# Performance work log

Measured on AMD Instinct MI355X. Metric: run time of the kernel, lower is better.

The kernel has to match this reference:

```python
import jax, jax.numpy as jnp
import numpy as np

BS, M, CLIP_DIM = 64, 1000, 512
D = 512
N_WAYS = 20
N_Z = 8


def setup_inputs() -> dict:
    key = jax.random.key(0)
    ks = jax.random.split(key, 16)
    s = 0.02
    inp = {
        "x_context": jax.random.normal(ks[0], (BS, M, CLIP_DIM), jnp.float32),
        "y_context": jax.random.randint(ks[1], (BS, M), 0, N_WAYS),
        "x_query": jax.random.normal(ks[2], (BS, M, CLIP_DIM), jnp.float32),
        # image_proj
        "Wp": jax.random.normal(ks[3], (CLIP_DIM, D), jnp.float32) * s,
        "bp": jnp.zeros((D,), jnp.float32),
        # aggregator: Linear(d,d) -> GELU -> Linear(d,2d)
        "Wa1": jax.random.normal(ks[4], (D, D), jnp.float32) * s,
        "ba1": jnp.zeros((D,), jnp.float32),
        "Wa2": jax.random.normal(ks[5], (D, 2 * D), jnp.float32) * s,
        "ba2": jnp.zeros((2 * D,), jnp.float32),
        # decoder: Linear(d,d) -> GELU -> Linear(d,d)
        "Wd1": jax.random.normal(ks[6], (D, D), jnp.float32) * s,
        "bd1": jnp.zeros((D,), jnp.float32),
        "Wd2": jax.random.normal(ks[7], (D, D), jnp.float32) * s,
        "bd2": jnp.zeros((D,), jnp.float32),
    }
    return inp


def reference(x_context, y_context, x_query, Wp, bp, Wa1, ba1, Wa2, ba2, Wd1, bd1, Wd2, bd2):
    # project image embeddings: [bs, M, clip_dim] -> [bs, M, d]
    xc = x_context @ Wp + bp
    xq = x_query @ Wp + bp

    # encode_context_per_class: per-class masked sum == one-hot segment-sum
    # (original loops over classes doing (x*mask).sum(dim=1))
    oh = jax.nn.one_hot(y_context, N_WAYS, dtype=xc.dtype)  # [bs, M, N]
    r_C = jnp.einsum('bmn,bmd->bnd', oh, xc)  # [bs, N, d]

    # knowledge is None -> k = zeros; combined = relu(r + 0)
    combined = jax.nn.relu(r_C)
    h = jax.nn.gelu(combined @ Wa1 + ba1, approximate=False)
    stats = h @ Wa2 + ba2  # [bs, N, 2d]
    mu, scale_raw = stats[..., :D], stats[..., D:]
    scale = 0.01 + 0.99 * jax.nn.softplus(scale_raw)

    # eval path: sample n_z from q(z|C) via reparameterization
    eps = jax.random.normal(jax.random.key(42), (N_Z,) + mu.shape, mu.dtype)
    z_samples = mu[None] + scale[None] * eps  # [n_z, bs, N, d]

    # decode: class weight vectors then inner product with queries
    W = jax.nn.gelu(z_samples @ Wd1 + bd1, approximate=False) @ Wd2 + bd2
    logits = jnp.einsum('bqd,sbnd->sbqn', xq, W)  # [n_z, bs, Q*N, N]
    return logits, z_samples, mu, scale
```

## Files before the change

### kernel.cpp

```cpp
#include <hip/hip_runtime.h>
#include <hip/hip_bf16.h>
#include <stdint.h>


typedef __attribute__((ext_vector_type(8))) short short8;
typedef __attribute__((ext_vector_type(4))) float f32x4;

__device__ __forceinline__ float gelu_f(float x) {
    return 0.5f * x * (1.0f + erff(x * 0.70710678118654752440f));
}
__device__ __forceinline__ float softplus_f(float x) {
    return fmaxf(x, 0.0f) + log1pf(expf(-fabsf(x)));
}
__device__ __forceinline__ uint32_t cvt2(float a, float b) {
    __hip_bfloat162 h;
    h.x = __float2bfloat16(a);
    h.y = __float2bfloat16(b);
    uint32_t u; __builtin_memcpy(&u, &h, 4); return u;
}
__device__ __forceinline__ unsigned short f2bfu(float f) {
    __hip_bfloat16 h = __float2bfloat16(f);
    unsigned short u; __builtin_memcpy(&u, &h, 2); return u;
}
__device__ __forceinline__ float bfu2f(unsigned short u) {
    uint32_t v = (uint32_t)u << 16; float f; __builtin_memcpy(&f, &v, 4); return f;
}

__device__ __forceinline__ void threefry2x32(uint32_t k0, uint32_t k1,
                                             uint32_t x0, uint32_t x1,
                                             uint32_t& o0, uint32_t& o1) {
    uint32_t ks[3] = {k0, k1, k0 ^ k1 ^ 0x1BD11BDAu};
    x0 += ks[0]; x1 += ks[1];
    const uint32_t rot[8] = {13,15,26,6,17,29,16,24};
#pragma unroll
    for (int i = 0; i < 5; i++) {
#pragma unroll
        for (int j = 0; j < 4; j++) {
            uint32_t r = rot[(i & 1) * 4 + j];
            x0 += x1;
            x1 = (x1 << r) | (x1 >> (32 - r));
            x1 ^= x0;
        }
        x0 += ks[(i + 1) % 3];
        x1 += ks[(i + 2) % 3] + (uint32_t)(i + 1);
    }
    o0 = x0; o1 = x1;
}

__device__ __forceinline__ float bits_to_normal(uint32_t b) {
    float f = __uint_as_float((b >> 9) | 0x3F800000u) - 1.0f;
    const float lo = __uint_as_float(0xBF7FFFFFu);
    float u = fmaxf(lo, f * 2.0f + lo);
    return 1.41421356237309504880f * erfinvf(u);
}

__global__ __launch_bounds__(256) void prep_k(
    const float* __restrict__ Wp, const float* __restrict__ Wa1,
    const float* __restrict__ Wa2, const float* __restrict__ Wd1,
    const float* __restrict__ Wd2, const float* __restrict__ bp,
    const float* __restrict__ bd2, const int* __restrict__ y,
    unsigned short* __restrict__ WpTb, unsigned short* __restrict__ Wa1Tb,
    unsigned short* __restrict__ Wa2Tb, unsigned short* __restrict__ WdT1b,
    float* __restrict__ bv, float* __restrict__ w2bp,
    float* __restrict__ c0, float* __restrict__ cnt)
{
    __shared__ float T[64][65];
    __shared__ int lc[32];
    __shared__ float ws4[4];
    const int f = blockIdx.x;
    const int tid = threadIdx.x;

    if (f < 320) {
        const float* src; unsigned short* dst; int C, t, xb, yb;
        if (f < 64)       { src = Wp;  dst = WpTb;  C = 512;  t = f;       xb = t & 7;  yb = t >> 3; }
        else if (f < 128) { src = Wa1; dst = Wa1Tb; C = 512;  t = f - 64;  xb = t & 7;  yb = t >> 3; }
        else if (f < 256) { src = Wa2; dst = Wa2Tb; C = 1024; t = f - 128; xb = t & 15; yb = t >> 4; }
        else              { src = Wd1; dst = WdT1b; C = 512;  t = f - 256; xb = t & 7;  yb = t >> 3; }
        const int r0 = yb * 64, cc0 = xb * 64;
        const int rr = tid >> 4, cc = (tid & 15) * 4;
#pragma unroll
        for (int l = 0; l < 4; l++) {
            int row = rr + l * 16;
            float4 v = *(const float4*)&src[(size_t)(r0 + row) * C + cc0 + cc];
            T[row][cc] = v.x; T[row][cc+1] = v.y; T[row][cc+2] = v.z; T[row][cc+3] = v.w;
        }
        __syncthreads();
#pragma unroll
        for (int l = 0; l < 4; l++) {
            int n = rr + l * 16;
            uint2 u;
            u.x = cvt2(T[cc][n], T[cc+1][n]);
            u.y = cvt2(T[cc+2][n], T[cc+3][n]);
            *(uint2*)&dst[(size_t)(cc0 + n) * 512 + r0 + cc] = u;
        }
    } else if (f < 576) {
        const float* W = (f < 448) ? Wp : Wd2;
        const float* v = (f < 448) ? bd2 : bp;
        float* o = (f < 448) ? bv : w2bp;
        int t = (f < 448) ? f - 320 : f - 448;
        int wave = tid >> 6, lane = tid & 63;
        int r = t * 4 + wave;
        const float* row = W + (size_t)r * 512 + lane * 8;
        float4 x0 = *(const float4*)row;
        float4 x1 = *(const float4*)(row + 4);
        float4 v0 = *(const float4*)&v[lane * 8];
        float4 v1 = *(const float4*)&v[lane * 8 + 4];
        float s = x0.x*v0.x + x0.y*v0.y + x0.z*v0.z + x0.w*v0.w
                + x1.x*v1.x + x1.y*v1.y + x1.z*v1.z + x1.w*v1.w;
#pragma unroll
        for (int off = 32; off > 0; off >>= 1) s += __shfl_down(s, off, 64);
        if (lane == 0) o[r] = s;
    } else if (f == 576) {
        float s = bp[tid] * bd2[tid] + bp[tid + 256] * bd2[tid + 256];
#pragma unroll
        for (int off = 32; off > 0; off >>= 1) s += __shfl_down(s, off, 64);
        int wave = tid >> 6, lane = tid & 63;
        if (lane == 0) ws4[wave] = s;
        __syncthreads();
        if (tid == 0) c0[0] = ws4[0] + ws4[1] + ws4[2] + ws4[3];
    } else {
        int b = f - 577;
        if (tid < 32) lc[tid] = 0;
        __syncthreads();
        for (int m = tid; m < 1000; m += 256)
            atomicAdd(&lc[y[b * 1000 + m]], 1);
        __syncthreads();
        if (tid < 20) cnt[b * 20 + tid] = (float)lc[tid];
    }
}

__global__ __launch_bounds__(256) void gmG_k(const float* __restrict__ Ap,
                                             const float* __restrict__ Bp,
                                             unsigned short* __restrict__ C) {
    __shared__ unsigned short As[64 * 64];
    __shared__ unsigned short Bs[128 * 64];
    const int tid = threadIdx.x;
    const int lane = tid & 63, w = tid >> 6;
    const int row0 = blockIdx.y * 64, col0 = blockIdx.x * 128;
    f32x4 acc[4][2] = {};
    for (int k0 = 0; k0 < 512; k0 += 64) {
        {
            int row = tid >> 2, cs = (tid & 3) * 16;
            int swz = (row & 7) << 4;
            const float* src = Ap + (size_t)(row0 + row) * 512 + k0 + cs;
#pragma unroll
            for (int j = 0; j < 2; j++) {
                float4 v0 = *(const float4*)(src + j * 8);
                float4 v1 = *(const float4*)(src + j * 8 + 4);
                uint4 u;
                u.x = cvt2(v0.x, v0.y); u.y = cvt2(v0.z, v0.w);
                u.z = cvt2(v1.x, v1.y); u.w = cvt2(v1.z, v1.w);
                *(uint4*)((char*)As + row * 128 + (((cs + j * 8) * 2) ^ swz)) = u;
            }
        }
        {
            int row = tid >> 1, cs = (tid & 1) * 32;
            int swz = (row & 7) << 4;
            const float* src = Bp + (size_t)(col0 + row) * 512 + k0 + cs;
#pragma unroll
            for (int j = 0; j < 4; j++) {
                float4 v0 = *(const float4*)(src + j * 8);
                float4 v1 = *(const float4*)(src + j * 8 + 4);
                uint4 u;
                u.x = cvt2(v0.x, v0.y); u.y = cvt2(v0.z, v0.w);
                u.z = cvt2(v1.x, v1.y); u.w = cvt2(v1.z, v1.w);
                *(uint4*)((char*)Bs + row * 128 + (((cs + j * 8) * 2) ^ swz)) = u;
            }
        }
        __syncthreads();
#pragma unroll
        for (int ks = 0; ks < 2; ks++) {
            short8 a[4], bb[2];
#pragma unroll
            for (int mi = 0; mi < 4; mi++) {
                int r = mi * 16 + (lane & 15);
                a[mi] = *(const short8*)((const char*)As + r * 128 +
                          (((ks * 32 + (lane >> 4) * 8) * 2) ^ ((r & 7) << 4)));
            }
#pragma unroll
            for (int ni = 0; ni < 2; ni++) {
                int n = w * 32 + ni * 16 + (lane & 15);
                bb[ni] = *(const short8*)((const char*)Bs + n * 128 +
                          (((ks * 32 + (lane >> 4) * 8) * 2) ^ ((n & 7) << 4)));
            }
#pragma unroll
            for (int mi = 0; mi < 4; mi++)
#pragma unroll
                for (int ni = 0; ni < 2; ni++)
                    acc[mi][ni] = __builtin_amdgcn_mfma_f32_16x16x32_bf16(a[mi], bb[ni], acc[mi][ni], 0, 0, 0);
        }
        __syncthreads();
    }
#pragma unroll
    for (int mi = 0; mi < 4; mi++)
#pragma unroll
        for (int ni = 0; ni < 2; ni++) {
            int c = col0 + w * 32 + ni * 16 + (lane & 15);
#pragma unroll
            for (int j = 0; j < 4; j++) {
                int r = row0 + mi * 16 + (lane >> 4) * 4 + j;
                C[(size_t)r * 512 + c] = f2bfu(acc[mi][ni][j]);
            }
        }
}

__global__ __launch_bounds__(256) void onehot4_k(const float* __restrict__ xc,
                                                 const int* __restrict__ y,
                                                 float* __restrict__ Apart) {
    __shared__ unsigned short Xs[128 * 64];
    __shared__ int ys[256];
    const int chb = blockIdx.x * 128;
    const int mc = blockIdx.y;
    const int b = blockIdx.z;
    const int m00 = mc * 256;
    const int tid = threadIdx.x, lane = tid & 63, w = tid >> 6;
    const int chs = w * 32;

    {
        int mg = m00 + tid;
        ys[tid] = (mg < 1000) ? y[b * 1000 + mg] : -1;
    }

    f32x4 acc[2][2] = {};
    for (int step = 0; step < 4; step++) {
        const int k0 = step * 64;
        int m = m00 + k0 + lane; if (m > 999) m = 999;
        const float* src = xc + ((size_t)b * 1000 + m) * 512 + chb + chs;
        float x[32];
#pragma unroll
        for (int j8 = 0; j8 < 8; j8++) {
            float4 v = *(const float4*)(src + j8 * 4);
            x[j8*4+0]=v.x; x[j8*4+1]=v.y; x[j8*4+2]=v.z; x[j8*4+3]=v.w;
        }
        __syncthreads();
#pragma unroll
        for (int j = 0; j < 32; j++) {
            int ch = chs + j;
            *(unsigned short*)((char*)Xs + ch * 128 + ((lane * 2) ^ ((ch & 7) << 4)))
                = f2bfu(x[j]);
        }
        __syncthreads();
#pragma unroll
        for (int ks = 0; ks < 2; ks++) {
            int kb = ks * 32 + (lane >> 4) * 8;
            int4 yv0 = *(const int4*)&ys[k0 + kb];
            int4 yv1 = *(const int4*)&ys[k0 + kb + 4];
            int ya[8] = {yv0.x, yv0.y, yv0.z, yv0.w, yv1.x, yv1.y, yv1.z, yv1.w};
            short8 a[2];
#pragma unroll
            for (int mi = 0; mi < 2; mi++) {
                int cls = mi * 16 + (lane & 15);
#pragma unroll
                for (int e = 0; e < 8; e++)
                    a[mi][e] = (short)((ya[e] == cls) ? 0x3F80 : 0);
            }
            short8 bb[2];
#pragma unroll
            for (int ni = 0; ni < 2; ni++) {
                int ch = chs + ni * 16 + (lane & 15);
                bb[ni] = *(const short8*)((const char*)Xs + ch * 128 +
                           ((kb * 2) ^ ((ch & 7) << 4)));
            }
#pragma unroll
            for (int mi = 0; mi < 2; mi++)
#pragma unroll
                for (int ni = 0; ni < 2; ni++)
                    acc[mi][ni] = __builtin_amdgcn_mfma_f32_16x16x32_bf16(a[mi], bb[ni], acc[mi][ni], 0, 0, 0);
        }
    }
    float* dst = Apart + (size_t)mc * 655360;
#pragma unroll
    for (int mi = 0; mi < 2; mi++) {
#pragma unroll
        for (int ni = 0; ni < 2; ni++) {
            int ch = chb + chs + ni * 16 + (lane & 15);
#pragma unroll
            for (int j = 0; j < 4; j++) {
                int cls = mi * 16 + (lane >> 4) * 4 + j;
                if (cls < 20)
                    dst[((size_t)b * 20 + cls) * 512 + ch] = acc[mi][ni][j];
            }
        }
    }
}

__global__ __launch_bounds__(256) void reduceA_k(const float* __restrict__ Apart,
                                                 unsigned short* __restrict__ Abf) {
    int i = blockIdx.x * 256 + threadIdx.x;
    if (i < 163840) {
        const float4* Ap4 = (const float4*)Apart;
        float4 s = Ap4[i];
#pragma unroll
        for (int p = 1; p < 4; p++) {
            float4 v = Ap4[(size_t)p * 163840 + i];
            s.x += v.x; s.y += v.y; s.z += v.z; s.w += v.w;
        }
        uint2 o;
        o.x = cvt2(s.x, s.y); o.y = cvt2(s.z, s.w);
        *(uint2*)&Abf[(size_t)i * 4] = o;
    }
}

template <int EPI>
__global__ __launch_bounds__(256) void gm2_k(const unsigned short* __restrict__ Abf,
                                             const unsigned short* __restrict__ Bbf,
                                             const float* __restrict__ bias,
                                             const float* __restrict__ extra,
                                             unsigned short* __restrict__ C0,
                                             float* __restrict__ F0,
                                             float* __restrict__ F1,
                                             int Nn) {
    __shared__ unsigned short As[64 * 64];
    __shared__ unsigned short Bs[128 * 64];
    const int tid = threadIdx.x;
    const int lane = tid & 63, w = tid >> 6;
    const int row0 = blockIdx.y * 64, col0 = blockIdx.x * 128;
    f32x4 acc[4][2] = {};
    for (int k0 = 0; k0 < 512; k0 += 64) {
        {
            int row = tid >> 2, cs = (tid & 3) * 16;
            int swz = (row & 7) << 4;
            const unsigned short* src = Abf + (size_t)(row0 + row) * 512 + k0 + cs;
#pragma unroll
            for (int j = 0; j < 2; j++) {
                uint4 u = *(const uint4*)(src + j * 8);
                *(uint4*)((char*)As + row * 128 + (((cs + j * 8) * 2) ^ swz)) = u;
            }
        }
        {
            int row = tid >> 1, cs = (tid & 1) * 32;
            int swz = (row & 7) << 4;
            const unsigned short* src = Bbf + (size_t)(col0 + row) * 512 + k0 + cs;
#pragma unroll
            for (int j = 0; j < 4; j++) {
                uint4 u = *(const uint4*)(src + j * 8);
                *(uint4*)((char*)Bs + row * 128 + (((cs + j * 8) * 2) ^ swz)) = u;
            }
        }
        __syncthreads();
#pragma unroll
        for (int ks = 0; ks < 2; ks++) {
            short8 a[4], bb[2];
#pragma unroll
            for (int mi = 0; mi < 4; mi++) {
                int r = mi * 16 + (lane & 15);
                a[mi] = *(const short8*)((const char*)As + r * 128 +
                          (((ks * 32 + (lane >> 4) * 8) * 2) ^ ((r & 7) << 4)));
            }
#pragma unroll
            for (int ni = 0; ni < 2; ni++) {
                int n = w * 32 + ni * 16 + (lane & 15);
                bb[ni] = *(const short8*)((const char*)Bs + n * 128 +
                          (((ks * 32 + (lane >> 4) * 8) * 2) ^ ((n & 7) << 4)));
            }
#pragma unroll
            for (int mi = 0; mi < 4; mi++)
#pragma unroll
                for (int ni = 0; ni < 2; ni++)
                    acc[mi][ni] = __builtin_amdgcn_mfma_f32_16x16x32_bf16(a[mi], bb[ni], acc[mi][ni], 0, 0, 0);
        }
        __syncthreads();
    }
#pragma unroll
    for (int mi = 0; mi < 4; mi++) {
#pragma unroll
        for (int ni = 0; ni < 2; ni++) {
            int c = col0 + w * 32 + ni * 16 + (lane & 15);
            float bvv = bias ? bias[c] : 0.f;
#pragma unroll
            for (int j = 0; j < 4; j++) {
                int r = row0 + mi * 16 + (lane >> 4) * 4 + j;
                float v = acc[mi][ni][j];
                if (EPI == 0) {
                    v += bvv;
                    C0[(size_t)r * Nn + c] = f2bfu(v);
                } else if (EPI == 1) {
                    v += extra[r] * bvv;
                    C0[(size_t)r * Nn + c] = f2bfu(fmaxf(v, 0.f));
                } else if (EPI == 2) {
                    C0[(size_t)r * Nn + c] = f2bfu(gelu_f(v + bvv));
                } else {
                    v += bvv;
                    if (c < 512) F0[(size_t)r * 512 + c] = v;
                    else F1[(size_t)r * 512 + (c - 512)] = 0.01f + 0.99f * softplus_f(v);
                }
            }
        }
    }
}

__global__ __launch_bounds__(256) void z2_k(const float* __restrict__ mu,
                                            const float* __restrict__ sc,
                                            float* __restrict__ z,
                                            unsigned short* __restrict__ zb) {
    const uint32_t NH = 2621440u;
    uint32_t i = blockIdx.x * 256u + threadIdx.x;
    if (i >= NH) return;
    uint32_t t0 = 2u * i;
    uint32_t o0, o1, p0, p1;
    threefry2x32(0u, 42u, 0u, t0, o0, o1);
    threefry2x32(0u, 42u, 0u, t0 + 1u, p0, p1);
    uint32_t r0 = t0 % 655360u;
    float2 mv = *(const float2*)&mu[r0];
    float2 sv = *(const float2*)&sc[r0];
    float z0 = mv.x + sv.x * bits_to_normal(o0 ^ o1);
    float z1 = mv.y + sv.y * bits_to_normal(p0 ^ p1);
    float2 zo; zo.x = z0; zo.y = z1;
    *(float2*)&z[t0] = zo;
    *(uint32_t*)&zb[t0] = cvt2(z0, z1);
}

__global__ __launch_bounds__(256) void beta2_k(const unsigned short* __restrict__ Wgb,
                                               const float* __restrict__ vec,
                                               const float* __restrict__ c0,
                                               float* __restrict__ beta) {
    int wave = threadIdx.x >> 6, lane = threadIdx.x & 63;
    int r = blockIdx.x * 4 + wave;
    short8 wv = *(const short8*)(Wgb + (size_t)r * 512 + lane * 8);
    float s = 0.f;
#pragma unroll
    for (int e = 0; e < 8; e++) s += vec[lane * 8 + e] * bfu2f((unsigned short)wv[e]);
#pragma unroll
    for (int o = 32; o > 0; o >>= 1) s += __shfl_down(s, o, 64);
    if (lane == 0) beta[r] = s + c0[0];
}

__global__ __launch_bounds__(512) void logits_mfma3_k(const float* __restrict__ Xq,
                                                      const unsigned short* __restrict__ Vb,
                                                      const float* __restrict__ beta,
                                                      float* __restrict__ out) {
    __shared__ unsigned short Vs[160 * 64];
    __shared__ float bs[160];
    const int u = blockIdx.x + 8 * blockIdx.y;
    const int xcd = u & 7, idx = u >> 3;
    const int b = (idx & 7) * 8 + xcd;
    const int qh = idx >> 3;
    const int tid = threadIdx.x, lane = tid & 63, w = tid >> 6;
    const int wq = w >> 1, wn = w & 1;

    if (tid < 160) {
        int s = tid / 20, n = tid - s * 20;
        bs[tid] = beta[(size_t)(s * 64 + b) * 20 + n];
    }

    const int klane = (lane >> 4) * 8;
    const float* xp[2];
    int qb[2];
#pragma unroll
    for (int qs = 0; qs < 2; qs++) {
        qb[qs] = qh * 128 + wq * 32 + qs * 16;
        int qr = qb[qs] + (lane & 15);
        if (qr > 999) qr = 999;
        xp[qs] = Xq + ((size_t)b * 1000 + qr) * 512 + klane;
    }
    int vrow[5], vswz[5];
#pragma unroll
    for (int nf = 0; nf < 5; nf++) {
        int rr = wn * 80 + nf * 16 + (lane & 15);
        vrow[nf] = rr * 128;
        vswz[nf] = (rr & 7) << 4;
    }

    f32x4 acc[2][5] = {};
    for (int k0 = 0; k0 < 512; k0 += 64) {
        __syncthreads();
        for (int c = tid; c < 640; c += 512) {
            int row = c >> 2, off = (c & 3) * 32;
            int sdiv = row / 20;
            int row_g = row + sdiv * 1260 + b * 20;
            const unsigned short* src = Vb + (size_t)row_g * 512 + k0 + (c & 3) * 16;
            uint4 u0 = *(const uint4*)src;
            uint4 u1 = *(const uint4*)(src + 8);
            int swz = (row & 7) << 4;
            char* base = (char*)Vs + row * 128;
            *(uint4*)(base + (off ^ swz)) = u0;
            *(uint4*)(base + ((off + 16) ^ swz)) = u1;
        }
        __syncthreads();
#pragma unroll
        for (int ks = 0; ks < 2; ks++) {
            int kb = (ks * 32 + klane) * 2;
            short8 bf[5];
#pragma unroll
            for (int nf = 0; nf < 5; nf++)
                bf[nf] = *(const short8*)((const char*)Vs + vrow[nf] + (kb ^ vswz[nf]));
            short8 af[2];
#pragma unroll
            for (int qs = 0; qs < 2; qs++) {
                const float* p = xp[qs] + k0 + ks * 32;
                float4 v0 = *(const float4*)p;
                float4 v1 = *(const float4*)(p + 4);
                uint4 uu;
                uu.x = cvt2(v0.x, v0.y); uu.y = cvt2(v0.z, v0.w);
                uu.z = cvt2(v1.x, v1.y); uu.w = cvt2(v1.z, v1.w);
                __builtin_memcpy(&af[qs], &uu, 16);
            }
#pragma unroll
            for (int qs = 0; qs < 2; qs++)
#pragma unroll
                for (int nf = 0; nf < 5; nf++)
                    acc[qs][nf] = __builtin_amdgcn_mfma_f32_16x16x32_bf16(af[qs], bf[nf], acc[qs][nf], 0, 0, 0);
        }
    }

#pragma unroll
    for (int nf = 0; nf < 5; nf++) {
        int rl = wn * 80 + nf * 16 + (lane & 15);
        int s = rl / 20, n = rl - s * 20;
        float bb = bs[rl];
        size_t ob = (size_t)(s * 64 + b) * 20000;
#pragma unroll
        for (int qs = 0; qs < 2; qs++) {
#pragma unroll
            for (int j = 0; j < 4; j++) {
                int q = qb[qs] + (lane >> 4) * 4 + j;
                if (q < 1000)
                    out[ob + (size_t)q * 20 + n] = acc[qs][nf][j] + bb;
            }
        }
    }
}

extern "C" void kernel_launch(void* const* d_in, const int* in_sizes, int n_in,
                              void* d_out, int out_size, void* d_ws, size_t ws_size,
                              hipStream_t stream) {
    const float* x_context = (const float*)d_in[0];
    const int*   y_context = (const int*)d_in[1];
    const float* x_query   = (const float*)d_in[2];
    const float* Wp  = (const float*)d_in[3];
    const float* bp  = (const float*)d_in[4];
    const float* Wa1 = (const float*)d_in[5];
    const float* ba1 = (const float*)d_in[6];
    const float* Wa2 = (const float*)d_in[7];
    const float* ba2 = (const float*)d_in[8];
    const float* Wd1 = (const float*)d_in[9];
    const float* bd1 = (const float*)d_in[10];
    const float* Wd2 = (const float*)d_in[11];
    const float* bd2 = (const float*)d_in[12];

    float* out    = (float*)d_out;
    float* logits = out;
    float* z      = out + 10240000;
    float* mu     = out + 15482880;
    float* sc     = out + 16138240;

    float* ws   = (float*)d_ws;
    float* cnt  = ws;
    float* beta = cnt + 1280;
    float* bv   = beta + 10240;
    float* w2bp = bv + 512;
    float* c0   = w2bp + 512;
    unsigned short* WpTb  = (unsigned short*)(c0 + 63);
    unsigned short* Wa1Tb = WpTb + 262144;
    unsigned short* Wa2Tb = Wa1Tb + 262144;
    unsigned short* WdT1b = Wa2Tb + 524288;
    unsigned short* Gtb   = WdT1b + 262144;
    unsigned short* Abf   = Gtb + 262144;
    unsigned short* combb = Abf + 655360;
    unsigned short* hb    = combb + 655360;
    unsigned short* zb    = hb + 655360;
    unsigned short* Vbf   = zb + 5242880;
    float* big = (float*)(Vbf + 5242880);
    unsigned short* Wgb = (unsigned short*)big;

    prep_k<<<dim3(641), 256, 0, stream>>>(Wp, Wa1, Wa2, Wd1, Wd2, bp, bd2, y_context,
                                          WpTb, Wa1Tb, Wa2Tb, WdT1b,
                                          bv, w2bp, c0, cnt);
    gmG_k<<<dim3(4, 8), 256, 0, stream>>>(Wp, Wd2, Gtb);
    onehot4_k<<<dim3(4, 4, 64), 256, 0, stream>>>(x_context, y_context, big);
    reduceA_k<<<dim3(640), 256, 0, stream>>>(big, Abf);
    gm2_k<1><<<dim3(4, 20), 256, 0, stream>>>(Abf, WpTb, bp, cnt, combb, nullptr, nullptr, 512);
    gm2_k<2><<<dim3(4, 20), 256, 0, stream>>>(combb, Wa1Tb, ba1, nullptr, hb, nullptr, nullptr, 512);
    gm2_k<3><<<dim3(8, 20), 256, 0, stream>>>(hb, Wa2Tb, ba2, nullptr, nullptr, mu, sc, 1024);
    z2_k<<<dim3(10240), 256, 0, stream>>>(mu, sc, z, zb);
    gm2_k<2><<<dim3(4, 160), 256, 0, stream>>>(zb, WdT1b, bd1, nullptr, Wgb, nullptr, nullptr, 512);
    gm2_k<0><<<dim3(4, 160), 256, 0, stream>>>(Wgb, Gtb, bv, nullptr, Vbf, nullptr, nullptr, 512);
    beta2_k<<<dim3(2560), 256, 0, stream>>>(Wgb, w2bp, c0, beta);
    logits_mfma3_k<<<dim3(8, 64), 512, 0, stream>>>(x_query, Vbf, beta, logits);
}
```

Measured before the change: 236.0 us.

## Fuse gmG into prep, fold partial-sum reduce into GEMM, double-buffer logits V tiles

The Wp·Wd2 product GEMM now runs as extra blocks inside the prep kernel, and the reduceA kernel is removed. The first small-M GEMM now sums the four fp32 partials directly while staging its A tile. The small-M GEMMs use 32-row tiles so more blocks run across the 1280-row problems. The logits kernel double-buffers its V tile in shared memory, so the next k-slice loads while the current one is multiplied, which removes one barrier per step. Together these cut two launches and one intermediate round trip, at the cost of more shared memory and redundant partial reads per column block.

```diff
diff --git a/kernel.cpp b/kernel.cpp
--- a/kernel.cpp
+++ b/kernel.cpp
@@ -61,16 +61,18 @@
     const float* __restrict__ bd2, const int* __restrict__ y,
     unsigned short* __restrict__ WpTb, unsigned short* __restrict__ Wa1Tb,
     unsigned short* __restrict__ Wa2Tb, unsigned short* __restrict__ WdT1b,
+    unsigned short* __restrict__ Gtb,
     float* __restrict__ bv, float* __restrict__ w2bp,
     float* __restrict__ c0, float* __restrict__ cnt)
 {
-    __shared__ float T[64][65];
+    __shared__ __align__(16) char sm[24576];
     __shared__ int lc[32];
     __shared__ float ws4[4];
     const int f = blockIdx.x;
     const int tid = threadIdx.x;
 
     if (f < 320) {
+        float (*T)[65] = reinterpret_cast<float(*)[65]>(sm);
         const float* src; unsigned short* dst; int C, t, xb, yb;
         if (f < 64)       { src = Wp;  dst = WpTb;  C = 512;  t = f;       xb = t & 7;  yb = t >> 3; }
         else if (f < 128) { src = Wa1; dst = Wa1Tb; C = 512;  t = f - 64;  xb = t & 7;  yb = t >> 3; }
@@ -118,7 +120,7 @@
         if (lane == 0) ws4[wave] = s;
         __syncthreads();
         if (tid == 0) c0[0] = ws4[0] + ws4[1] + ws4[2] + ws4[3];
-    } else {
+    } else if (f < 641) {
         int b = f - 577;
         if (tid < 32) lc[tid] = 0;
         __syncthreads();
@@ -126,82 +128,78 @@
             atomicAdd(&lc[y[b * 1000 + m]], 1);
         __syncthreads();
         if (tid < 20) cnt[b * 20 + tid] = (float)lc[tid];
-    }
-}
-
-__global__ __launch_bounds__(256) void gmG_k(const float* __restrict__ Ap,
-                                             const float* __restrict__ Bp,
-                                             unsigned short* __restrict__ C) {
-    __shared__ unsigned short As[64 * 64];
-    __shared__ unsigned short Bs[128 * 64];
-    const int tid = threadIdx.x;
-    const int lane = tid & 63, w = tid >> 6;
-    const int row0 = blockIdx.y * 64, col0 = blockIdx.x * 128;
-    f32x4 acc[4][2] = {};
-    for (int k0 = 0; k0 < 512; k0 += 64) {
-        {
-            int row = tid >> 2, cs = (tid & 3) * 16;
-            int swz = (row & 7) << 4;
-            const float* src = Ap + (size_t)(row0 + row) * 512 + k0 + cs;
-#pragma unroll
-            for (int j = 0; j < 2; j++) {
-                float4 v0 = *(const float4*)(src + j * 8);
-                float4 v1 = *(const float4*)(src + j * 8 + 4);
-                uint4 u;
-                u.x = cvt2(v0.x, v0.y); u.y = cvt2(v0.z, v0.w);
-                u.z = cvt2(v1.x, v1.y); u.w = cvt2(v1.z, v1.w);
-                *(uint4*)((char*)As + row * 128 + (((cs + j * 8) * 2) ^ swz)) = u;
-            }
-        }
-        {
-            int row = tid >> 1, cs = (tid & 1) * 32;
-            int swz = (row & 7) << 4;
-            const float* src = Bp + (size_t)(col0 + row) * 512 + k0 + cs;
-#pragma unroll
-            for (int j = 0; j < 4; j++) {
-                float4 v0 = *(const float4*)(src + j * 8);
-                float4 v1 = *(const float4*)(src + j * 8 + 4);
-                uint4 u;
-                u.x = cvt2(v0.x, v0.y); u.y = cvt2(v0.z, v0.w);
-                u.z = cvt2(v1.x, v1.y); u.w = cvt2(v1.z, v1.w);
-                *(uint4*)((char*)Bs + row * 128 + (((cs + j * 8) * 2) ^ swz)) = u;
-            }
-        }
-        __syncthreads();
-#pragma unroll
-        for (int ks = 0; ks < 2; ks++) {
-            short8 a[4], bb[2];
-#pragma unroll
-            for (int mi = 0; mi < 4; mi++) {
-                int r = mi * 16 + (lane & 15);
-                a[mi] = *(const short8*)((const char*)As + r * 128 +
-                          (((ks * 32 + (lane >> 4) * 8) * 2) ^ ((r & 7) << 4)));
-            }
+    } else {
+        unsigned short* As = (unsigned short*)sm;
+        unsigned short* Bs = (unsigned short*)(sm + 8192);
+        const int g = f - 641;
+        const int lane = tid & 63, w = tid >> 6;
+        const int row0 = (g >> 2) * 64, col0 = (g & 3) * 128;
+        f32x4 acc[4][2] = {};
+        for (int k0 = 0; k0 < 512; k0 += 64) {
+            {
+                int row = tid >> 2, cs = (tid & 3) * 16;
+                int swz = (row & 7) << 4;
+                const float* src = Wp + (size_t)(row0 + row) * 512 + k0 + cs;
+#pragma unroll
+                for (int j = 0; j < 2; j++) {
+                    float4 v0 = *(const float4*)(src + j * 8);
+                    float4 v1 = *(const float4*)(src + j * 8 + 4);
+                    uint4 u;
+                    u.x = cvt2(v0.x, v0.y); u.y = cvt2(v0.z, v0.w);
+                    u.z = cvt2(v1.x, v1.y); u.w = cvt2(v1.z, v1.w);
+                    *(uint4*)((char*)As + row * 128 + (((cs + j * 8) * 2) ^ swz)) = u;
+                }
+            }
+            {
+                int row = tid >> 1, cs = (tid & 1) * 32;
+                int swz = (row & 7) << 4;
+                const float* src = Wd2 + (size_t)(col0 + row) * 512 + k0 + cs;
+#pragma unroll
+                for (int j = 0; j < 4; j++) {
+                    float4 v0 = *(const float4*)(src + j * 8);
+                    float4 v1 = *(const float4*)(src + j * 8 + 4);
+                    uint4 u;
+                    u.x = cvt2(v0.x, v0.y); u.y = cvt2(v0.z, v0.w);
+                    u.z = cvt2(v1.x, v1.y); u.w = cvt2(v1.z, v1.w);
+                    *(uint4*)((char*)Bs + row * 128 + (((cs + j * 8) * 2) ^ swz)) = u;
+                }
+            }
+            __syncthreads();
+#pragma unroll
+            for (int ks = 0; ks < 2; ks++) {
+                short8 a[4], bb[2];
+#pragma unroll
+                for (int mi = 0; mi < 4; mi++) {
+                    int r = mi * 16 + (lane & 15);
+                    a[mi] = *(const short8*)((const char*)As + r * 128 +
+                              (((ks * 32 + (lane >> 4) * 8) * 2) ^ ((r & 7) << 4)));
+                }
+#pragma unroll
+                for (int ni = 0; ni < 2; ni++) {
+                    int n = w * 32 + ni * 16 + (lane & 15);
+                    bb[ni] = *(const short8*)((const char*)Bs + n * 128 +
+                              (((ks * 32 + (lane >> 4) * 8) * 2) ^ ((n & 7) << 4)));
+                }
+#pragma unroll
+                for (int mi = 0; mi < 4; mi++)
+#pragma unroll
+                    for (int ni = 0; ni < 2; ni++)
+                        acc[mi][ni] = __builtin_amdgcn_mfma_f32_16x16x32_bf16(a[mi], bb[ni], acc[mi][ni], 0, 0, 0);
+            }
+            __syncthreads();
+        }
+#pragma unroll
+        for (int mi = 0; mi < 4; mi++)
 #pragma unroll
             for (int ni = 0; ni < 2; ni++) {
-                int n = w * 32 + ni * 16 + (lane & 15);
-                bb[ni] = *(const short8*)((const char*)Bs + n * 128 +
-                          (((ks * 32 + (lane >> 4) * 8) * 2) ^ ((n & 7) << 4)));
-            }
-#pragma unroll
-            for (int mi = 0; mi < 4; mi++)
-#pragma unroll
-                for (int ni = 0; ni < 2; ni++)
-                    acc[mi][ni] = __builtin_amdgcn_mfma_f32_16x16x32_bf16(a[mi], bb[ni], acc[mi][ni], 0, 0, 0);
-        }
-        __syncthreads();
-    }
-#pragma unroll
-    for (int mi = 0; mi < 4; mi++)
-#pragma unroll
-        for (int ni = 0; ni < 2; ni++) {
-            int c = col0 + w * 32 + ni * 16 + (lane & 15);
-#pragma unroll
-            for (int j = 0; j < 4; j++) {
-                int r = row0 + mi * 16 + (lane >> 4) * 4 + j;
-                C[(size_t)r * 512 + c] = f2bfu(acc[mi][ni][j]);
-            }
-        }
+                int c = col0 + w * 32 + ni * 16 + (lane & 15);
+#pragma unroll
+                for (int j = 0; j < 4; j++) {
+                    int r = row0 + mi * 16 + (lane >> 4) * 4 + j;
+                    Gtb[(size_t)r * 512 + c] = f2bfu(acc[mi][ni][j]);
+                }
+            }
+    }
 }
 
 __global__ __launch_bounds__(256) void onehot4_k(const float* __restrict__ xc,
@@ -284,24 +282,7 @@
     }
 }
 
-__global__ __launch_bounds__(256) void reduceA_k(const float* __restrict__ Apart,
-                                                 unsigned short* __restrict__ Abf) {
-    int i = blockIdx.x * 256 + threadIdx.x;
-    if (i < 163840) {
-        const float4* Ap4 = (const float4*)Apart;
-        float4 s = Ap4[i];
-#pragma unroll
-        for (int p = 1; p < 4; p++) {
-            float4 v = Ap4[(size_t)p * 163840 + i];
-            s.x += v.x; s.y += v.y; s.z += v.z; s.w += v.w;
-        }
-        uint2 o;
-        o.x = cvt2(s.x, s.y); o.y = cvt2(s.z, s.w);
-        *(uint2*)&Abf[(size_t)i * 4] = o;
-    }
-}
-
-template <int EPI>
+template <int EPI, int MT, int A4>
 __global__ __launch_bounds__(256) void gm2_k(const unsigned short* __restrict__ Abf,
                                              const unsigned short* __restrict__ Bbf,
                                              const float* __restrict__ bias,
@@ -310,14 +291,14 @@
                                              float* __restrict__ F0,
                                              float* __restrict__ F1,
                                              int Nn) {
-    __shared__ unsigned short As[64 * 64];
+    __shared__ unsigned short As[MT * 64];
     __shared__ unsigned short Bs[128 * 64];
     const int tid = threadIdx.x;
     const int lane = tid & 63, w = tid >> 6;
-    const int row0 = blockIdx.y * 64, col0 = blockIdx.x * 128;
-    f32x4 acc[4][2] = {};
+    const int row0 = blockIdx.y * MT, col0 = blockIdx.x * 128;
+    f32x4 acc[MT / 16][2] = {};
     for (int k0 = 0; k0 < 512; k0 += 64) {
-        {
+        if constexpr (MT == 64) {
             int row = tid >> 2, cs = (tid & 3) * 16;
             int swz = (row & 7) << 4;
             const unsigned short* src = Abf + (size_t)(row0 + row) * 512 + k0 + cs;
@@ -326,6 +307,27 @@
                 uint4 u = *(const uint4*)(src + j * 8);
                 *(uint4*)((char*)As + row * 128 + (((cs + j * 8) * 2) ^ swz)) = u;
             }
+        } else {
+            int row = tid >> 3, cs = (tid & 7) * 8;
+            int swz = (row & 7) << 4;
+            uint4 u;
+            if constexpr (A4) {
+                const float* p = (const float*)Abf + (size_t)(row0 + row) * 512 + k0 + cs;
+                float4 s0 = *(const float4*)p;
+                float4 s1 = *(const float4*)(p + 4);
+#pragma unroll
+                for (int q = 1; q < 4; q++) {
+                    const float* pp = p + (size_t)q * 655360;
+                    float4 v0 = *(const float4*)pp, v1 = *(const float4*)(pp + 4);
+                    s0.x += v0.x; s0.y += v0.y; s0.z += v0.z; s0.w += v0.w;
+                    s1.x += v1.x; s1.y += v1.y; s1.z += v1.z; s1.w += v1.w;
+                }
+                u.x = cvt2(s0.x, s0.y); u.y = cvt2(s0.z, s0.w);
+                u.z = cvt2(s1.x, s1.y); u.w = cvt2(s1.z, s1.w);
+            } else {
+                u = *(const uint4*)(Abf + (size_t)(row0 + row) * 512 + k0 + cs);
+            }
+            *(uint4*)((char*)As + row * 128 + ((cs * 2) ^ swz)) = u;
         }
         {
             int row = tid >> 1, cs = (tid & 1) * 32;
@@ -340,9 +342,9 @@
         __syncthreads();
 #pragma unroll
         for (int ks = 0; ks < 2; ks++) {
-            short8 a[4], bb[2];
-#pragma unroll
-            for (int mi = 0; mi < 4; mi++) {
+            short8 a[MT / 16], bb[2];
+#pragma unroll
+            for (int mi = 0; mi < MT / 16; mi++) {
                 int r = mi * 16 + (lane & 15);
                 a[mi] = *(const short8*)((const char*)As + r * 128 +
                           (((ks * 32 + (lane >> 4) * 8) * 2) ^ ((r & 7) << 4)));
@@ -354,7 +356,7 @@
                           (((ks * 32 + (lane >> 4) * 8) * 2) ^ ((n & 7) << 4)));
             }
 #pragma unroll
-            for (int mi = 0; mi < 4; mi++)
+            for (int mi = 0; mi < MT / 16; mi++)
 #pragma unroll
                 for (int ni = 0; ni < 2; ni++)
                     acc[mi][ni] = __builtin_amdgcn_mfma_f32_16x16x32_bf16(a[mi], bb[ni], acc[mi][ni], 0, 0, 0);
@@ -362,7 +364,7 @@
         __syncthreads();
     }
 #pragma unroll
-    for (int mi = 0; mi < 4; mi++) {
+    for (int mi = 0; mi < MT / 16; mi++) {
 #pragma unroll
         for (int ni = 0; ni < 2; ni++) {
             int c = col0 + w * 32 + ni * 16 + (lane & 15);
@@ -425,11 +427,11 @@
     if (lane == 0) beta[r] = s + c0[0];
 }
 
-__global__ __launch_bounds__(512) void logits_mfma3_k(const float* __restrict__ Xq,
+__global__ __launch_bounds__(512) void logits_mfma4_k(const float* __restrict__ Xq,
                                                       const unsigned short* __restrict__ Vb,
                                                       const float* __restrict__ beta,
                                                       float* __restrict__ out) {
-    __shared__ unsigned short Vs[160 * 64];
+    __shared__ unsigned short Vs[2][160 * 64];
     __shared__ float bs[160];
     const int u = blockIdx.x + 8 * blockIdx.y;
     const int xcd = u & 7, idx = u >> 3;
@@ -443,27 +445,7 @@
         bs[tid] = beta[(size_t)(s * 64 + b) * 20 + n];
     }
 
-    const int klane = (lane >> 4) * 8;
-    const float* xp[2];
-    int qb[2];
-#pragma unroll
-    for (int qs = 0; qs < 2; qs++) {
-        qb[qs] = qh * 128 + wq * 32 + qs * 16;
-        int qr = qb[qs] + (lane & 15);
-        if (qr > 999) qr = 999;
-        xp[qs] = Xq + ((size_t)b * 1000 + qr) * 512 + klane;
-    }
-    int vrow[5], vswz[5];
-#pragma unroll
-    for (int nf = 0; nf < 5; nf++) {
-        int rr = wn * 80 + nf * 16 + (lane & 15);
-        vrow[nf] = rr * 128;
-        vswz[nf] = (rr & 7) << 4;
-    }
-
-    f32x4 acc[2][5] = {};
-    for (int k0 = 0; k0 < 512; k0 += 64) {
-        __syncthreads();
+    auto stageV = [&](int buf, int k0) {
         for (int c = tid; c < 640; c += 512) {
             int row = c >> 2, off = (c & 3) * 32;
             int sdiv = row / 20;
@@ -472,18 +454,46 @@
             uint4 u0 = *(const uint4*)src;
             uint4 u1 = *(const uint4*)(src + 8);
             int swz = (row & 7) << 4;
-            char* base = (char*)Vs + row * 128;
+            char* base = (char*)&Vs[buf][0] + row * 128;
             *(uint4*)(base + (off ^ swz)) = u0;
             *(uint4*)(base + ((off + 16) ^ swz)) = u1;
         }
-        __syncthreads();
+    };
+
+    const int klane = (lane >> 4) * 8;
+    const float* xp[2];
+    int qb[2];
+#pragma unroll
+    for (int qs = 0; qs < 2; qs++) {
+        qb[qs] = qh * 128 + wq * 32 + qs * 16;
+        int qr = qb[qs] + (lane & 15);
+        if (qr > 999) qr = 999;
+        xp[qs] = Xq + ((size_t)b * 1000 + qr) * 512 + klane;
+    }
+    int vrow[5], vswz[5];
+#pragma unroll
+    for (int nf = 0; nf < 5; nf++) {
+        int rr = wn * 80 + nf * 16 + (lane & 15);
+        vrow[nf] = rr * 128;
+        vswz[nf] = (rr & 7) << 4;
+    }
+
+    stageV(0, 0);
+    __syncthreads();
+
+    f32x4 acc[2][5] = {};
+    int cur = 0;
+    for (int step = 0; step < 8; step++) {
+        const int k0 = step * 64;
+        if (step < 7) stageV(cur ^ 1, k0 + 64);
+        const char* vbase = (const char*)&Vs[cur][0];
 #pragma unroll
         for (int ks = 0; ks < 2; ks++) {
             int kb = (ks * 32 + klane) * 2;
             short8 bf[5];
 #pragma unroll
             for (int nf = 0; nf < 5; nf++)
-                bf[nf] = *(const short8*)((const char*)Vs + vrow[nf] + (kb ^ vswz[nf]));
+                bf[nf] = *(const short8*)(vbase + vrow[nf] + (kb ^ vswz[nf]));
             short8 af[2];
 #pragma unroll
             for (int qs = 0; qs < 2; qs++) {
@@ -501,6 +511,8 @@
                 for (int nf = 0; nf < 5; nf++)
                     acc[qs][nf] = __builtin_amdgcn_mfma_f32_16x16x32_bf16(af[qs], bf[nf], acc[qs][nf], 0, 0, 0);
         }
+        __syncthreads();
+        cur ^= 1;
     }
 
 #pragma unroll
@@ -555,26 +567,23 @@
     unsigned short* Wa2Tb = Wa1Tb + 262144;
     unsigned short* WdT1b = Wa2Tb + 524288;
     unsigned short* Gtb   = WdT1b + 262144;
-    unsigned short* Abf   = Gtb + 262144;
-    unsigned short* combb = Abf + 655360;
+    unsigned short* combb = Gtb + 262144;
     unsigned short* hb    = combb + 655360;
     unsigned short* zb    = hb + 655360;
     unsigned short* Vbf   = zb + 5242880;
     float* big = (float*)(Vbf + 5242880);
     unsigned short* Wgb = (unsigned short*)big;
 
-    prep_k<<<dim3(641), 256, 0, stream>>>(Wp, Wa1, Wa2, Wd1, Wd2, bp, bd2, y_context,
-                                          WpTb, Wa1Tb, Wa2Tb, WdT1b,
+    prep_k<<<dim3(673), 256, 0, stream>>>(Wp, Wa1, Wa2, Wd1, Wd2, bp, bd2, y_context,
+                                          WpTb, Wa1Tb, Wa2Tb, WdT1b, Gtb,
                                           bv, w2bp, c0, cnt);
-    gmG_k<<<dim3(4, 8), 256, 0, stream>>>(Wp, Wd2, Gtb);
     onehot4_k<<<dim3(4, 4, 64), 256, 0, stream>>>(x_context, y_context, big);
-    reduceA_k<<<dim3(640), 256, 0, stream>>>(big, Abf);
-    gm2_k<1><<<dim3(4, 20), 256, 0, stream>>>(Abf, WpTb, bp, cnt, combb, nullptr, nullptr, 512);
-    gm2_k<2><<<dim3(4, 20), 256, 0, stream>>>(combb, Wa1Tb, ba1, nullptr, hb, nullptr, nullptr, 512);
-    gm2_k<3><<<dim3(8, 20), 256, 0, stream>>>(hb, Wa2Tb, ba2, nullptr, nullptr, mu, sc, 1024);
+    gm2_k<1, 32, 1><<<dim3(4, 40), 256, 0, stream>>>((const unsigned short*)big, WpTb, bp, cnt, combb, nullptr, nullptr, 512);
+    gm2_k<2, 32, 0><<<dim3(4, 40), 256, 0, stream>>>(combb, Wa1Tb, ba1, nullptr, hb, nullptr, nullptr, 512);
+    gm2_k<3, 32, 0><<<dim3(8, 40), 256, 0, stream>>>(hb, Wa2Tb, ba2, nullptr, nullptr, mu, sc, 1024);
     z2_k<<<dim3(10240), 256, 0, stream>>>(mu, sc, z, zb);
-    gm2_k<2><<<dim3(4, 160), 256, 0, stream>>>(zb, WdT1b, bd1, nullptr, Wgb, nullptr, nullptr, 512);
-    gm2_k<0><<<dim3(4, 160), 256, 0, stream>>>(Wgb, Gtb, bv, nullptr, Vbf, nullptr, nullptr, 512);
+    gm2_k<2, 64, 0><<<dim3(4, 160), 256, 0, stream>>>(zb, WdT1b, bd1, nullptr, Wgb, nullptr, nullptr, 512);
+    gm2_k<0, 64, 0><<<dim3(4, 160), 256, 0, stream>>>(Wgb, Gtb, bv, nullptr, Vbf, nullptr, nullptr, 512);
     beta2_k<<<dim3(2560), 256, 0, stream>>>(Wgb, w2bp, c0, beta);
-    logits_mfma3_k<<<dim3(8, 64), 512, 0, stream>>>(x_query, Vbf, beta, logits);
-}
+    logits_mfma4_k<<<dim3(8, 64), 512, 0, stream>>>(x_query, Vbf, beta, logits);
+}
```

New measurement: 224.2 us. 5.0% less time.
